# Kernel optimization log

Hardware: AMD Instinct MI355X
Metric: run time of the kernel (lower is better)

The kernel has to match this reference:

```python
import jax, jax.numpy as jnp
import numpy as np
import itertools

DIMS = (128, 128, 128)
CHANNELS = 8
BATCH = 2_097_152


def setup_inputs() -> dict:
    key = jax.random.key(0)
    k1, k2 = jax.random.split(key)
    unList = jax.random.uniform(k1, (BATCH, len(DIMS)), dtype=jnp.float32)
    table = jax.random.uniform(k2, DIMS + (CHANNELS,), dtype=jnp.float32)  # initScale=1, initMode='R'
    return {"unList": unList, "table": table}


def reference(unList, table):
    # N-D multilinear (bilinear/trilinear) interpolated table lookup.
    dims = table.shape[:-1]
    n = len(dims)
    c = table.shape[-1]
    dims_f = jnp.asarray(dims, jnp.float32)
    # map normalized coords [0,1] onto grid [0, dim-1]
    scaled = jnp.clip(unList, 0.0, 1.0) * (dims_f - 1.0)          # [B, n]
    i0 = jnp.clip(jnp.floor(scaled), 0.0, dims_f - 2.0).astype(jnp.int32)  # lower corner
    frac = scaled - i0.astype(jnp.float32)                        # [B, n] in [0,1]
    # flatten grid for single-axis gathers
    strides = jnp.asarray([int(np.prod(dims[k + 1:])) for k in range(n)], jnp.int32)
    table_flat = table.reshape(-1, c)                             # [prod(dims), C]
    out = jnp.zeros((unList.shape[0], c), table.dtype)
    # loop over the 2^n corners (8 for 3D) -- small static loop
    for corner in itertools.product((0, 1), repeat=n):
        bits = jnp.asarray(corner, jnp.int32)                     # [n]
        flat_idx = ((i0 + bits) * strides).sum(-1)                # [B]
        w = jnp.prod(jnp.where(jnp.asarray(corner, bool), frac, 1.0 - frac), axis=-1)  # [B]
        out = out + w[:, None] * table_flat[flat_idx]             # gather + weighted sum
    return out
```

## Files before the change

### kernel.cpp

```cpp
#include <hip/hip_runtime.h>


#define DIM 128
#define CH 8
#define NBIN 2048
#define TBYTES 67108864u
#define CHUNK 8192
#define PPT 32
#define SLAB 61440
#define CUR_OFF 8192
#define BASE_OFF 16384
#define REC_OFF 32768

__device__ __forceinline__ int key_of(float ux, float uy) {
    float sx = fminf(fmaxf(ux, 0.0f), 1.0f) * 127.0f;
    float sy = fminf(fmaxf(uy, 0.0f), 1.0f) * 127.0f;
    int x0 = (int)fminf(floorf(sx), 126.0f);
    int y0 = (int)fminf(floorf(sy), 126.0f);
    return (x0 >> 1) * 32 + (y0 >> 2);
}

__global__ __launch_bounds__(256) void k_hist(const float* __restrict__ un,
                                              unsigned* __restrict__ hist, int batch) {
    __shared__ unsigned lh[NBIN];
    for (int i = threadIdx.x; i < NBIN; i += 256) lh[i] = 0;
    __syncthreads();
    int stride = gridDim.x * blockDim.x;
    for (int i = blockIdx.x * blockDim.x + threadIdx.x; i < batch; i += stride)
        atomicAdd(&lh[key_of(un[3 * i], un[3 * i + 1])], 1u);
    __syncthreads();
    for (int i = threadIdx.x; i < NBIN; i += 256)
        if (lh[i]) atomicAdd(&hist[i], lh[i]);
}

__global__ __launch_bounds__(1024) void k_scan(const unsigned* __restrict__ hist,
                                               unsigned* __restrict__ cursor,
                                               unsigned* __restrict__ base) {
    __shared__ unsigned s[1024];
    int t = threadIdx.x;
    unsigned h0 = hist[t * 2], h1 = hist[t * 2 + 1];
    s[t] = h0 + h1;
    __syncthreads();
    for (int off = 1; off < 1024; off <<= 1) {
        unsigned v = (t >= off) ? s[t - off] : 0u;
        __syncthreads();
        s[t] += v;
        __syncthreads();
    }
    unsigned excl = s[t] - (h0 + h1);
    base[t * 2] = excl;           cursor[t * 2] = excl;
    base[t * 2 + 1] = excl + h0;  cursor[t * 2 + 1] = excl + h0;
    if (t == 1023) base[NBIN] = s[1023];
}

__global__ __launch_bounds__(256) void k_scatter(const float* __restrict__ un,
                                                 unsigned* __restrict__ cursor,
                                                 uint2* __restrict__ rec, int batch) {
    __shared__ unsigned lh[NBIN];
    __shared__ unsigned lbase[NBIN];
    int t = threadIdx.x;
    for (int i = t; i < NBIN; i += 256) lh[i] = 0;
    __syncthreads();
    int start = blockIdx.x * CHUNK;
    unsigned kr[PPT];
#pragma unroll
    for (int j = 0; j < PPT; ++j) {
        int i = start + j * 256 + t;
        if (i < batch) {
            int k = key_of(un[3 * i], un[3 * i + 1]);
            unsigned r = atomicAdd(&lh[k], 1u);
            kr[j] = (unsigned)k | (r << 12);
        } else kr[j] = 0u;
    }
    __syncthreads();
    for (int i = t; i < NBIN; i += 256)
        lbase[i] = lh[i] ? atomicAdd(&cursor[i], lh[i]) : 0u;
    __syncthreads();
#pragma unroll
    for (int j = 0; j < PPT; ++j) {
        int i = start + j * 256 + t;
        if (i < batch) {
            unsigned k = kr[j] & 4095u, r = kr[j] >> 12;
            float ux = un[3 * i], uy = un[3 * i + 1], uz = un[3 * i + 2];
            float sx = fminf(fmaxf(ux, 0.0f), 1.0f) * 127.0f;
            float sy = fminf(fmaxf(uy, 0.0f), 1.0f) * 127.0f;
            float sz = fminf(fmaxf(uz, 0.0f), 1.0f) * 127.0f;
            float fx0 = fminf(floorf(sx), 126.0f);
            float fy0 = fminf(floorf(sy), 126.0f);
            float fz0 = fminf(floorf(sz), 126.0f);
            int x0 = (int)fx0, y0 = (int)fy0, z0 = (int)fz0;
            unsigned qx = (unsigned)((sx - fx0) * 2047.0f + 0.5f);
            unsigned qy = (unsigned)((sy - fy0) * 2047.0f + 0.5f);
            unsigned qz = (unsigned)((sz - fz0) * 1023.0f + 0.5f);
            unsigned dx = (unsigned)(x0 & 1);
            unsigned dy = (unsigned)(y0 & 3);
            uint2 rr;
            rr.x = (unsigned)i | (dx << 21) | (dy << 22) | ((unsigned)z0 << 24);
            rr.y = qx | (qy << 11) | (qz << 22);
            rec[lbase[k] + r] = rr;
        }
    }
}

__global__ __launch_bounds__(512, 4) void k_main(const uint2* __restrict__ rec,
                                                 const float* __restrict__ table,
                                                 const unsigned* __restrict__ base,
                                                 float* __restrict__ out) {
    __shared__ float4 lds4[SLAB / 16];
    char* ldsb = (char*)lds4;
    const char* tb = (const char*)table;

    int pb = (int)blockIdx.x;
    int g = (pb & 7) * 256 + (pb >> 3);
    int X = g >> 5, Y = g & 31;
    unsigned s = base[g], e = base[g + 1];

    int t = (int)threadIdx.x;
    int lane = t & 63, wave = t >> 6;

#pragma unroll
    for (int j = 0; j < 8; ++j) {
        int c = wave + j * 8;
        if (c < 60) {
            int pr = c >> 2, q4 = c & 3;
            int p = (pr * 13) >> 6;
            int r = pr - p * 5;
            int gp = 2 * X + p;  if (gp > 127) gp = 127;
            int gr = 4 * Y + r;  if (gr > 127) gr = 127;
            unsigned go = (unsigned)((gp * 128 + gr) * 4096 + q4 * 1024)
                        + (unsigned)lane * 16u;
            __builtin_amdgcn_global_load_lds(
                (const __attribute__((address_space(1))) void*)(tb + go),
                (__attribute__((address_space(3))) void*)(ldsb + (unsigned)c * 1024u),
                16, 0, 0);
        }
    }
    __syncthreads();
    if (e <= s) return;

    int p = lane >> 1, h = lane & 1;
    const unsigned hoff = (unsigned)(h << 4);
    const unsigned last = e - 1u;
    const float rs11 = 1.0f / 2047.0f, rs10 = 1.0f / 1023.0f;

    unsigned myi = s + (unsigned)(wave * 32 + p);
    unsigned cnt = e - s;

#define PROC(rr, idx) { \
        if ((idx) < e) { \
            unsigned orig = rr.x & 0x1FFFFFu; \
            unsigned dx = (rr.x >> 21) & 1u; \
            unsigned dy = (rr.x >> 22) & 3u; \
            unsigned z0 = (rr.x >> 24) & 0x7Fu; \
            float fx = (float)(rr.y & 0x7FFu) * rs11; \
            float fy = (float)((rr.y >> 11) & 0x7FFu) * rs11; \
            float fz = (float)(rr.y >> 22) * rs10; \
            float gxw = 1.0f - fx, gyw = 1.0f - fy, gzw = 1.0f - fz; \
            float wA0 = gxw * gyw * gzw, wA1 = gxw * gyw * fz; \
            float wB0 = gxw * fy  * gzw, wB1 = gxw * fy  * fz; \
            float wC0 = fx  * gyw * gzw, wC1 = fx  * gyw * fz; \
            float wD0 = fx  * fy  * gzw, wD1 = fx  * fy  * fz; \
            unsigned a = (dx * 5u + dy) * 4096u + z0 * 32u + hoff; \
            float4 vA0 = *(const float4*)(ldsb + a); \
            float4 vA1 = *(const float4*)(ldsb + a + 32u); \
            float4 vB0 = *(const float4*)(ldsb + a + 4096u); \
            float4 vB1 = *(const float4*)(ldsb + a + 4128u); \
            float4 vC0 = *(const float4*)(ldsb + a + 20480u); \
            float4 vC1 = *(const float4*)(ldsb + a + 20512u); \
            float4 vD0 = *(const float4*)(ldsb + a + 24576u); \
            float4 vD1 = *(const float4*)(ldsb + a + 24608u); \
            float4 acc; \
            acc.x = wA0*vA0.x + wA1*vA1.x + wB0*vB0.x + wB1*vB1.x \
                  + wC0*vC0.x + wC1*vC1.x + wD0*vD0.x + wD1*vD1.x; \
            acc.y = wA0*vA0.y + wA1*vA1.y + wB0*vB0.y + wB1*vB1.y \
                  + wC0*vC0.y + wC1*vC1.y + wD0*vD0.y + wD1*vD1.y; \
            acc.z = wA0*vA0.z + wA1*vA1.z + wB0*vB0.z + wB1*vB1.z \
                  + wC0*vC0.z + wC1*vC1.z + wD0*vD0.z + wD1*vD1.z; \
            acc.w = wA0*vA0.w + wA1*vA1.w + wB0*vB0.w + wB1*vB1.w \
                  + wC0*vC0.w + wC1*vC1.w + wD0*vD0.w + wD1*vD1.w; \
            *reinterpret_cast<float4*>(out + (size_t)orig * CH + (h << 2)) = acc; \
        } }

    uint2 r0 = rec[min(myi, last)];
    for (unsigned c0 = 0; c0 < cnt; c0 += 256u) {
        uint2 n0 = rec[min(myi + c0 + 256u, last)];
        PROC(r0, myi + c0)
        r0 = n0;
    }
#undef PROC
}

__global__ __launch_bounds__(256) void k_naive(const float* __restrict__ un,
                                               const float* __restrict__ table,
                                               float* __restrict__ out, int batch) {
    int b = blockIdx.x * blockDim.x + threadIdx.x;
    if (b >= batch) return;
    float ux = un[3 * b], uy = un[3 * b + 1], uz = un[3 * b + 2];
    const float dmax = 127.0f, imax = 126.0f;
    float sx = fminf(fmaxf(ux, 0.0f), 1.0f) * dmax;
    float sy = fminf(fmaxf(uy, 0.0f), 1.0f) * dmax;
    float sz = fminf(fmaxf(uz, 0.0f), 1.0f) * dmax;
    float fx0 = fminf(floorf(sx), imax);
    float fy0 = fminf(floorf(sy), imax);
    float fz0 = fminf(floorf(sz), imax);
    int x0 = (int)fx0, y0 = (int)fy0, z0 = (int)fz0;
    float fx = sx - fx0, fy = sy - fy0, fz = sz - fz0;
    float wx[2] = {1.0f - fx, fx};
    float wy[2] = {1.0f - fy, fy};
    float wz0 = 1.0f - fz, wz1 = fz;
    float acc[CH];
#pragma unroll
    for (int c = 0; c < CH; ++c) acc[c] = 0.0f;
#pragma unroll
    for (int bx = 0; bx < 2; ++bx)
#pragma unroll
        for (int by = 0; by < 2; ++by) {
            const float* pp = table + ((size_t)((x0 + bx) * DIM + (y0 + by)) * DIM + z0) * CH;
            float wxy = wx[bx] * wy[by];
            float w0 = wxy * wz0, w1 = wxy * wz1;
            float4 a0 = *reinterpret_cast<const float4*>(pp + 0);
            float4 a1 = *reinterpret_cast<const float4*>(pp + 4);
            float4 b0 = *reinterpret_cast<const float4*>(pp + 8);
            float4 b1 = *reinterpret_cast<const float4*>(pp + 12);
            acc[0] += w0 * a0.x + w1 * b0.x;  acc[1] += w0 * a0.y + w1 * b0.y;
            acc[2] += w0 * a0.z + w1 * b0.z;  acc[3] += w0 * a0.w + w1 * b0.w;
            acc[4] += w0 * a1.x + w1 * b1.x;  acc[5] += w0 * a1.y + w1 * b1.y;
            acc[6] += w0 * a1.z + w1 * b1.z;  acc[7] += w0 * a1.w + w1 * b1.w;
        }
    float4* o = reinterpret_cast<float4*>(out + (size_t)b * CH);
    o[0] = make_float4(acc[0], acc[1], acc[2], acc[3]);
    o[1] = make_float4(acc[4], acc[5], acc[6], acc[7]);
}

extern "C" void kernel_launch(void* const* d_in, const int* in_sizes, int n_in,
                              void* d_out, int out_size, void* d_ws, size_t ws_size,
                              hipStream_t stream) {
    const float* un    = (const float*)d_in[0];
    const float* table = (const float*)d_in[1];
    float* out         = (float*)d_out;
    int batch = in_sizes[0] / 3;

    size_t need = (size_t)REC_OFF + (size_t)batch * 8;
    if (ws_size < need || batch > (1 << 21)) {
        int grid = (batch + 255) / 256;
        k_naive<<<grid, 256, 0, stream>>>(un, table, out, batch);
        return;
    }

    unsigned* hist   = (unsigned*)d_ws;
    unsigned* cursor = (unsigned*)((char*)d_ws + CUR_OFF);
    unsigned* base   = (unsigned*)((char*)d_ws + BASE_OFF);
    uint2*    rec    = (uint2*)((char*)d_ws + REC_OFF);

    hipMemsetAsync(d_ws, 0, CUR_OFF, stream);
    k_hist<<<512, 256, 0, stream>>>(un, hist, batch);
    k_scan<<<1, 1024, 0, stream>>>(hist, cursor, base);
    int nscat = (batch + CHUNK - 1) / CHUNK;
    k_scatter<<<nscat, 256, 0, stream>>>(un, cursor, rec, batch);
    k_main<<<NBIN, 512, 0, stream>>>(rec, table, base, out);
}
```

Baseline: 108.8 us.

## Process four bins per block with double-buffered LDS slab prefetch

The main kernel becomes a persistent-style loop in which each 1024-thread block handles four consecutive bins. The table slab for the next bin is loaded into a second LDS buffer with global_load_lds while the current bin is processed, which is meant to hide slab-load latency behind compute. LDS use per block doubles to about 120KB, which limits residency to one block per CU. The per-record prefetch of rec entries is dropped.

Result: no change. 110.5 us (+1.6%).

```diff
diff --git a/kernel.cpp b/kernel.cpp
--- a/kernel.cpp
+++ b/kernel.cpp
@@ -7,7 +7,8 @@
 #define TBYTES 67108864u
 #define CHUNK 8192
 #define PPT 32
-#define SLAB 61440
+#define SLABB 61440u
+#define BPB 4
 #define CUR_OFF 8192
 #define BASE_OFF 16384
 #define REC_OFF 32768
@@ -102,92 +103,93 @@
     }
 }
 
-__global__ __launch_bounds__(512, 4) void k_main(const uint2* __restrict__ rec,
-                                                 const float* __restrict__ table,
-                                                 const unsigned* __restrict__ base,
-                                                 float* __restrict__ out) {
-    __shared__ float4 lds4[SLAB / 16];
+__global__ __launch_bounds__(1024, 4) void k_main(const uint2* __restrict__ rec,
+                                                  const float* __restrict__ table,
+                                                  const unsigned* __restrict__ base,
+                                                  float* __restrict__ out) {
+    __shared__ float4 lds4[2 * SLABB / 16];
     char* ldsb = (char*)lds4;
     const char* tb = (const char*)table;
 
-    int pb = (int)blockIdx.x;
-    int g = (pb & 7) * 256 + (pb >> 3);
-    int X = g >> 5, Y = g & 31;
-    unsigned s = base[g], e = base[g + 1];
+    int b = (int)blockIdx.x;
+    int bb = (b & 7) * 64 + (b >> 3);
+    int g0 = bb * BPB;
 
     int t = (int)threadIdx.x;
     int lane = t & 63, wave = t >> 6;
-
-#pragma unroll
-    for (int j = 0; j < 8; ++j) {
-        int c = wave + j * 8;
-        if (c < 60) {
-            int pr = c >> 2, q4 = c & 3;
-            int p = (pr * 13) >> 6;
-            int r = pr - p * 5;
-            int gp = 2 * X + p;  if (gp > 127) gp = 127;
-            int gr = 4 * Y + r;  if (gr > 127) gr = 127;
-            unsigned go = (unsigned)((gp * 128 + gr) * 4096 + q4 * 1024)
-                        + (unsigned)lane * 16u;
-            __builtin_amdgcn_global_load_lds(
-                (const __attribute__((address_space(1))) void*)(tb + go),
-                (__attribute__((address_space(3))) void*)(ldsb + (unsigned)c * 1024u),
-                16, 0, 0);
-        }
-    }
-    __syncthreads();
-    if (e <= s) return;
-
     int p = lane >> 1, h = lane & 1;
     const unsigned hoff = (unsigned)(h << 4);
-    const unsigned last = e - 1u;
     const float rs11 = 1.0f / 2047.0f, rs10 = 1.0f / 1023.0f;
 
-    unsigned myi = s + (unsigned)(wave * 32 + p);
-    unsigned cnt = e - s;
-
-#define PROC(rr, idx) { \
-        if ((idx) < e) { \
-            unsigned orig = rr.x & 0x1FFFFFu; \
-            unsigned dx = (rr.x >> 21) & 1u; \
-            unsigned dy = (rr.x >> 22) & 3u; \
-            unsigned z0 = (rr.x >> 24) & 0x7Fu; \
-            float fx = (float)(rr.y & 0x7FFu) * rs11; \
-            float fy = (float)((rr.y >> 11) & 0x7FFu) * rs11; \
-            float fz = (float)(rr.y >> 22) * rs10; \
-            float gxw = 1.0f - fx, gyw = 1.0f - fy, gzw = 1.0f - fz; \
-            float wA0 = gxw * gyw * gzw, wA1 = gxw * gyw * fz; \
-            float wB0 = gxw * fy  * gzw, wB1 = gxw * fy  * fz; \
-            float wC0 = fx  * gyw * gzw, wC1 = fx  * gyw * fz; \
-            float wD0 = fx  * fy  * gzw, wD1 = fx  * fy  * fz; \
-            unsigned a = (dx * 5u + dy) * 4096u + z0 * 32u + hoff; \
-            float4 vA0 = *(const float4*)(ldsb + a); \
-            float4 vA1 = *(const float4*)(ldsb + a + 32u); \
-            float4 vB0 = *(const float4*)(ldsb + a + 4096u); \
-            float4 vB1 = *(const float4*)(ldsb + a + 4128u); \
-            float4 vC0 = *(const float4*)(ldsb + a + 20480u); \
-            float4 vC1 = *(const float4*)(ldsb + a + 20512u); \
-            float4 vD0 = *(const float4*)(ldsb + a + 24576u); \
-            float4 vD1 = *(const float4*)(ldsb + a + 24608u); \
-            float4 acc; \
-            acc.x = wA0*vA0.x + wA1*vA1.x + wB0*vB0.x + wB1*vB1.x \
-                  + wC0*vC0.x + wC1*vC1.x + wD0*vD0.x + wD1*vD1.x; \
-            acc.y = wA0*vA0.y + wA1*vA1.y + wB0*vB0.y + wB1*vB1.y \
-                  + wC0*vC0.y + wC1*vC1.y + wD0*vD0.y + wD1*vD1.y; \
-            acc.z = wA0*vA0.z + wA1*vA1.z + wB0*vB0.z + wB1*vB1.z \
-                  + wC0*vC0.z + wC1*vC1.z + wD0*vD0.z + wD1*vD1.z; \
-            acc.w = wA0*vA0.w + wA1*vA1.w + wB0*vB0.w + wB1*vB1.w \
-                  + wC0*vC0.w + wC1*vC1.w + wD0*vD0.w + wD1*vD1.w; \
-            *reinterpret_cast<float4*>(out + (size_t)orig * CH + (h << 2)) = acc; \
+#define STAGE(binid, buf) { \
+        int X_ = (binid) >> 5, Y_ = (binid) & 31; \
+        _Pragma("unroll") \
+        for (int k_ = 0; k_ < 4; ++k_) { \
+            int c_ = wave + k_ * 16; \
+            if (c_ < 60) { \
+                int pr_ = c_ >> 2, q4_ = c_ & 3; \
+                int p2_ = (pr_ * 13) >> 6; \
+                int r2_ = pr_ - p2_ * 5; \
+                int gp_ = 2 * X_ + p2_;  if (gp_ > 127) gp_ = 127; \
+                int gr_ = 4 * Y_ + r2_;  if (gr_ > 127) gr_ = 127; \
+                unsigned go_ = (unsigned)((gp_ * 128 + gr_) * 4096 + q4_ * 1024) \
+                             + (unsigned)lane * 16u; \
+                __builtin_amdgcn_global_load_lds( \
+                    (const __attribute__((address_space(1))) void*)(tb + go_), \
+                    (__attribute__((address_space(3))) void*)(ldsb + (buf) * SLABB \
+                        + (unsigned)c_ * 1024u), 16, 0, 0); \
+            } \
         } }
 
-    uint2 r0 = rec[min(myi, last)];
-    for (unsigned c0 = 0; c0 < cnt; c0 += 256u) {
-        uint2 n0 = rec[min(myi + c0 + 256u, last)];
-        PROC(r0, myi + c0)
-        r0 = n0;
-    }
-#undef PROC
+    STAGE(g0, 0u)
+
+    for (int j = 0; j < BPB; ++j) {
+        asm volatile("s_waitcnt vmcnt(0) lgkmcnt(0)" ::: "memory");
+        __builtin_amdgcn_s_barrier();
+        __builtin_amdgcn_sched_barrier(0);
+        if (j + 1 < BPB) STAGE(g0 + j + 1, (unsigned)((j + 1) & 1))
+        __builtin_amdgcn_sched_barrier(0);
+
+        unsigned s = base[g0 + j], e = base[g0 + j + 1];
+        const char* lb = ldsb + (unsigned)(j & 1) * SLABB;
+
+        for (unsigned idx = s + (unsigned)(wave * 32 + p); idx < e; idx += 512u) {
+            uint2 rr = rec[idx];
+            unsigned orig = rr.x & 0x1FFFFFu;
+            unsigned dx = (rr.x >> 21) & 1u;
+            unsigned dy = (rr.x >> 22) & 3u;
+            unsigned z0 = (rr.x >> 24) & 0x7Fu;
+            float fx = (float)(rr.y & 0x7FFu) * rs11;
+            float fy = (float)((rr.y >> 11) & 0x7FFu) * rs11;
+            float fz = (float)(rr.y >> 22) * rs10;
+            float gxw = 1.0f - fx, gyw = 1.0f - fy, gzw = 1.0f - fz;
+            float wA0 = gxw * gyw * gzw, wA1 = gxw * gyw * fz;
+            float wB0 = gxw * fy  * gzw, wB1 = gxw * fy  * fz;
+            float wC0 = fx  * gyw * gzw, wC1 = fx  * gyw * fz;
+            float wD0 = fx  * fy  * gzw, wD1 = fx  * fy  * fz;
+            unsigned a = (dx * 5u + dy) * 4096u + z0 * 32u + hoff;
+            float4 vA0 = *(const float4*)(lb + a);
+            float4 vA1 = *(const float4*)(lb + a + 32u);
+            float4 vB0 = *(const float4*)(lb + a + 4096u);
+            float4 vB1 = *(const float4*)(lb + a + 4128u);
+            float4 vC0 = *(const float4*)(lb + a + 20480u);
+            float4 vC1 = *(const float4*)(lb + a + 20512u);
+            float4 vD0 = *(const float4*)(lb + a + 24576u);
+            float4 vD1 = *(const float4*)(lb + a + 24608u);
+            float4 acc;
+            acc.x = wA0*vA0.x + wA1*vA1.x + wB0*vB0.x + wB1*vB1.x
+                  + wC0*vC0.x + wC1*vC1.x + wD0*vD0.x + wD1*vD1.x;
+            acc.y = wA0*vA0.y + wA1*vA1.y + wB0*vB0.y + wB1*vB1.y
+                  + wC0*vC0.y + wC1*vC1.y + wD0*vD0.y + wD1*vD1.y;
+            acc.z = wA0*vA0.z + wA1*vA1.z + wB0*vB0.z + wB1*vB1.z
+                  + wC0*vC0.z + wC1*vC1.z + wD0*vD0.z + wD1*vD1.z;
+            acc.w = wA0*vA0.w + wA1*vA1.w + wB0*vB0.w + wB1*vB1.w
+                  + wC0*vC0.w + wC1*vC1.w + wD0*vD0.w + wD1*vD1.w;
+            *reinterpret_cast<float4*>(out + (size_t)orig * CH + (h << 2)) = acc;
+        }
+        __builtin_amdgcn_sched_barrier(0);
+    }
+#undef STAGE
 }
 
 __global__ __launch_bounds__(256) void k_naive(const float* __restrict__ un,
@@ -257,5 +259,5 @@
     k_scan<<<1, 1024, 0, stream>>>(hist, cursor, base);
     int nscat = (batch + CHUNK - 1) / CHUNK;
     k_scatter<<<nscat, 256, 0, stream>>>(un, cursor, rec, batch);
-    k_main<<<NBIN, 512, 0, stream>>>(rec, table, base, out);
-}
+    k_main<<<NBIN / BPB, 1024, 0, stream>>>(rec, table, base, out);
+}
```
